# Kernel optimization log

Hardware: AMD Instinct MI355X
Metric: run time of the kernel (lower is better)

## Reference

```python
import jax, jax.numpy as jnp
import numpy as np


def setup_inputs() -> dict:
    key = jax.random.key(0)
    k1, k2 = jax.random.split(key)
    B, C, H, W = 16, 256, 96, 96
    x1 = jax.random.normal(k1, (B, C, H, W), dtype=jnp.float32)
    x2 = jax.random.normal(k2, (B, C, H, W), dtype=jnp.float32)
    return {"x1": x1, "x2": x2, "k": 1, "d": 4, "s1": 1, "s2": 1}


def reference(x1, x2, k, d, s1, s2):
    """FlowNet-style correlation cost volume (k=1 pointwise patch).

    out[b, i, y, x] = (1/(k*k*C)) * sum_c x1[b,c,y,x] * x2_pad[b,c,y+dy_i,x+dx_i]
    for displacements (dy, dx) in [-d, d] with stride s2 (x2 zero-padded by d).
    Output strided by s1 over spatial dims. Output channels = (2*d//s2 + 1)**2.
    """
    assert k == 1, "reference specialized to k=1 (pointwise correlation)"
    B, C, H, W = x1.shape
    norm = 1.0 / (k * k * C)
    # zero-pad x2 by max displacement d on each spatial side
    x2p = jnp.pad(x2, ((0, 0), (0, 0), (d, d), (d, d)))
    offsets = list(range(-d, d + 1, s2))  # displacement grid (fixed, small)
    outs = []
    for dy in offsets:
        for dx in offsets:
            shifted = x2p[:, :, d + dy:d + dy + H, d + dx:d + dx + W]  # [B,C,H,W]
            outs.append(jnp.einsum('bchw,bchw->bhw', x1, shifted) * norm)
    out = jnp.stack(outs, axis=1)  # [B, D*D, H, W]
    return out[:, :, ::s1, ::s1]
```

## Files before the change

### kernel.cpp

```cpp
#include <hip/hip_runtime.h>


namespace {
constexpr int Bsz = 16, Cch = 256, Hh = 96, Ww = 96;
constexpr int Dd = 4, NDisp = 9;
constexpr int TH = 4;
constexpr int PX = 8;
constexpr int NSTRIP = Ww / PX;
constexpr int CC = 4;
constexpr int X2ROWS = TH + 2 * Dd;
constexpr int X2P = 105;
constexpr int NT = TH * NDisp * NSTRIP;
constexpr int HW = Hh * Ww;
constexpr int X1_LDS = CC * TH * Ww;
constexpr int X2_LDS = CC * X2ROWS * X2P;
constexpr int X1_F4 = X1_LDS / 4;
constexpr int X2_GROUPS = 26;
constexpr int X2_F4 = CC * X2ROWS * X2_GROUPS;
constexpr int N_ITEMS = X1_F4 + X2_F4;
}

__global__ __launch_bounds__(NT, 2)
void corr81(const float* __restrict__ x1, const float* __restrict__ x2,
            float* __restrict__ out) {
  __shared__ float lds[X1_LDS + X2_LDS + 4];

  const int t = threadIdx.x;
  const int y0 = blockIdx.x * TH;
  const int b  = blockIdx.y;

  const int r   = t / (NDisp * NSTRIP);
  const int rem = t % (NDisp * NSTRIP);
  const int dyi = rem / NSTRIP;
  const int s   = rem % NSTRIP;
  const int x0  = s * PX;

  const float* __restrict__ x1b = x1 + (size_t)b * Cch * HW;
  const float* __restrict__ x2b = x2 + (size_t)b * Cch * HW;

  const float* gp[4];
  int  loff[4];
  bool zero[4];
#pragma unroll
  for (int j = 0; j < 4; ++j) {
    int i = t + j * NT;
    if (i >= N_ITEMS) {
      gp[j] = x1b; loff[j] = X1_LDS + X2_LDS; zero[j] = true;
    } else if (i < X1_F4) {
      int c = i / (TH * Ww / 4);
      int q = i % (TH * Ww / 4);
      gp[j]   = x1b + c * HW + y0 * Ww + q * 4;
      loff[j] = c * (TH * Ww) + q * 4;
      zero[j] = false;
    } else {
      int m  = i - X1_F4;
      int c  = m / (X2ROWS * X2_GROUPS);
      int m2 = m % (X2ROWS * X2_GROUPS);
      int ry = m2 / X2_GROUPS;
      int g  = m2 % X2_GROUPS;
      int gy = y0 + ry - Dd;
      bool z = (gy < 0) | (gy >= Hh) | (g == 0) | (g == X2_GROUPS - 1);
      gp[j]   = z ? x2b : (x2b + c * HW + gy * Ww + (g - 1) * 4);
      loff[j] = X1_LDS + c * (X2ROWS * X2P) + ry * X2P + g * 4;
      zero[j] = z;
    }
  }

  float acc[NDisp][PX];
#pragma unroll
  for (int i = 0; i < NDisp; ++i)
#pragma unroll
    for (int j = 0; j < PX; ++j) acc[i][j] = 0.f;

  float4 v[4];
#pragma unroll
  for (int j = 0; j < 4; ++j)
    v[j] = zero[j] ? make_float4(0.f, 0.f, 0.f, 0.f) : *(const float4*)gp[j];

  for (int c0 = 0; c0 < Cch; c0 += CC) {
    __syncthreads();
#pragma unroll
    for (int j = 0; j < 4; ++j) {
      int o = loff[j];
      if (o < X1_LDS) {
        *(float4*)(lds + o) = v[j];
      } else {
        lds[o] = v[j].x; lds[o + 1] = v[j].y; lds[o + 2] = v[j].z; lds[o + 3] = v[j].w;
      }
    }
    __syncthreads();
    if (c0 + CC < Cch) {
#pragma unroll
      for (int j = 0; j < 4; ++j) {
        gp[j] += CC * HW;
        v[j] = zero[j] ? make_float4(0.f, 0.f, 0.f, 0.f) : *(const float4*)gp[j];
      }
    }
#pragma unroll
    for (int cc = 0; cc < CC; ++cc) {
      const float* ap = lds + cc * (TH * Ww) + r * Ww + x0;
      float a[PX];
      *(float4*)(a)     = *(const float4*)(ap);
      *(float4*)(a + 4) = *(const float4*)(ap + 4);
      const float* bp = lds + X1_LDS + cc * (X2ROWS * X2P) + (r + dyi) * X2P + x0;
      float bb[PX + 2 * Dd];
#pragma unroll
      for (int q = 0; q < PX + 2 * Dd; ++q) bb[q] = bp[q];
#pragma unroll
      for (int dx = 0; dx < NDisp; ++dx)
#pragma unroll
        for (int px = 0; px < PX; ++px)
          acc[dx][px] += a[px] * bb[px + dx];
    }
  }

  const float nrm = 1.0f / (float)Cch;
  float* ob = out + ((size_t)b * (NDisp * NDisp) + (size_t)dyi * NDisp) * HW
                  + (size_t)(y0 + r) * Ww + x0;
#pragma unroll
  for (int dx = 0; dx < NDisp; ++dx) {
    float4 w0, w1;
    w0.x = acc[dx][0] * nrm; w0.y = acc[dx][1] * nrm;
    w0.z = acc[dx][2] * nrm; w0.w = acc[dx][3] * nrm;
    w1.x = acc[dx][4] * nrm; w1.y = acc[dx][5] * nrm;
    w1.z = acc[dx][6] * nrm; w1.w = acc[dx][7] * nrm;
    *(float4*)(ob + (size_t)dx * HW)     = w0;
    *(float4*)(ob + (size_t)dx * HW + 4) = w1;
  }
}

extern "C" void kernel_launch(void* const* d_in, const int* in_sizes, int n_in,
                              void* d_out, int out_size, void* d_ws, size_t ws_size,
                              hipStream_t stream) {
  const float* x1 = (const float*)d_in[0];
  const float* x2 = (const float*)d_in[1];
  float* out = (float*)d_out;
  dim3 grid(Hh / TH, Bsz);
  dim3 block(NT);
  hipLaunchKernelGGL(corr81, grid, block, 0, stream, x1, x2, out);
}
```

Before: 486.3 us.

## Pad LDS rows in 8-float chunks with stride 12 to enable vector loads

Restructures the shared-memory layout of the x1 and x2 tiles into 8-float chunks stored at a stride of 12 floats. The padded x2 row becomes 16-byte aligned, so both the staging stores and the 16-element window reads can use float4 accesses instead of scalar ones, while the padding is meant to reduce bank conflicts. It also raises the launch_bounds occupancy hint from 2 to 4 blocks, which may force register pressure or spills given the 72-float accumulator. The LDS footprint grows because of the padding.

Result: slower. 1.193 ms (+145.4%).

```diff
diff --git a/kernel.cpp b/kernel.cpp
--- a/kernel.cpp
+++ b/kernel.cpp
@@ -9,18 +9,24 @@
 constexpr int NSTRIP = Ww / PX;
 constexpr int CC = 4;
 constexpr int X2ROWS = TH + 2 * Dd;
-constexpr int X2P = 105;
 constexpr int NT = TH * NDisp * NSTRIP;
 constexpr int HW = Hh * Ww;
-constexpr int X1_LDS = CC * TH * Ww;
-constexpr int X2_LDS = CC * X2ROWS * X2P;
-constexpr int X1_F4 = X1_LDS / 4;
-constexpr int X2_GROUPS = 26;
+
+constexpr int CHUNK = 12;
+constexpr int X1CH  = Ww / 8;
+constexpr int X1RP  = X1CH * CHUNK;
+constexpr int X1_LDS = CC * TH * X1RP;
+constexpr int X2COLS = 104;
+constexpr int X2CH  = X2COLS / 8;
+constexpr int X2RP  = X2CH * CHUNK;
+constexpr int X2_LDS = CC * X2ROWS * X2RP;
+constexpr int X2_GROUPS = X2COLS / 4;
+constexpr int X1_F4 = CC * TH * Ww / 4;
 constexpr int X2_F4 = CC * X2ROWS * X2_GROUPS;
 constexpr int N_ITEMS = X1_F4 + X2_F4;
 }
 
-__global__ __launch_bounds__(NT, 2)
+__global__ __launch_bounds__(NT, 4)
 void corr81(const float* __restrict__ x1, const float* __restrict__ x2,
             float* __restrict__ out) {
   __shared__ float lds[X1_LDS + X2_LDS + 4];
@@ -47,10 +53,12 @@
     if (i >= N_ITEMS) {
       gp[j] = x1b; loff[j] = X1_LDS + X2_LDS; zero[j] = true;
     } else if (i < X1_F4) {
-      int c = i / (TH * Ww / 4);
-      int q = i % (TH * Ww / 4);
-      gp[j]   = x1b + c * HW + y0 * Ww + q * 4;
-      loff[j] = c * (TH * Ww) + q * 4;
+      int c    = i / (TH * Ww / 4);
+      int q    = i % (TH * Ww / 4);
+      int grow = q / (Ww / 4);
+      int col  = (q % (Ww / 4)) * 4;
+      gp[j]   = x1b + c * HW + (size_t)(y0 + grow) * Ww + col;
+      loff[j] = c * (TH * X1RP) + grow * X1RP + (col >> 3) * CHUNK + (col & 7);
       zero[j] = false;
     } else {
       int m  = i - X1_F4;
@@ -58,10 +66,12 @@
       int m2 = m % (X2ROWS * X2_GROUPS);
       int ry = m2 / X2_GROUPS;
       int g  = m2 % X2_GROUPS;
+      int pc = g * 4;
       int gy = y0 + ry - Dd;
       bool z = (gy < 0) | (gy >= Hh) | (g == 0) | (g == X2_GROUPS - 1);
-      gp[j]   = z ? x2b : (x2b + c * HW + gy * Ww + (g - 1) * 4);
-      loff[j] = X1_LDS + c * (X2ROWS * X2P) + ry * X2P + g * 4;
+      gp[j]   = z ? x2b : (x2b + c * HW + gy * Ww + (pc - 4));
+      loff[j] = X1_LDS + c * (X2ROWS * X2RP) + ry * X2RP
+              + (pc >> 3) * CHUNK + (pc & 7);
       zero[j] = z;
     }
   }
@@ -72,6 +82,9 @@
 #pragma unroll
     for (int j = 0; j < PX; ++j) acc[i][j] = 0.f;
 
+  const float* ap0 = lds + r * X1RP + s * CHUNK;
+  const float* bp0 = lds + X1_LDS + (r + dyi) * X2RP + s * CHUNK;
+
   float4 v[4];
 #pragma unroll
   for (int j = 0; j < 4; ++j)
@@ -80,14 +93,8 @@
   for (int c0 = 0; c0 < Cch; c0 += CC) {
     __syncthreads();
 #pragma unroll
-    for (int j = 0; j < 4; ++j) {
-      int o = loff[j];
-      if (o < X1_LDS) {
-        *(float4*)(lds + o) = v[j];
-      } else {
-        lds[o] = v[j].x; lds[o + 1] = v[j].y; lds[o + 2] = v[j].z; lds[o + 3] = v[j].w;
-      }
-    }
+    for (int j = 0; j < 4; ++j)
+      *(float4*)(lds + loff[j]) = v[j];
     __syncthreads();
     if (c0 + CC < Cch) {
 #pragma unroll
@@ -98,14 +105,16 @@
     }
 #pragma unroll
     for (int cc = 0; cc < CC; ++cc) {
-      const float* ap = lds + cc * (TH * Ww) + r * Ww + x0;
+      const float* ap = ap0 + cc * (TH * X1RP);
       float a[PX];
       *(float4*)(a)     = *(const float4*)(ap);
       *(float4*)(a + 4) = *(const float4*)(ap + 4);
-      const float* bp = lds + X1_LDS + cc * (X2ROWS * X2P) + (r + dyi) * X2P + x0;
+      const float* bp = bp0 + cc * (X2ROWS * X2RP);
       float bb[PX + 2 * Dd];
-#pragma unroll
-      for (int q = 0; q < PX + 2 * Dd; ++q) bb[q] = bp[q];
+      *(float4*)(bb)      = *(const float4*)(bp);
+      *(float4*)(bb + 4)  = *(const float4*)(bp + 4);
+      *(float4*)(bb + 8)  = *(const float4*)(bp + CHUNK);
+      *(float4*)(bb + 12) = *(const float4*)(bp + CHUNK + 4);
 #pragma unroll
       for (int dx = 0; dx < NDisp; ++dx)
 #pragma unroll
```
